# Performance work log

Hardware: AMD Instinct MI355X
Metric: run time of the kernel (lower is better)

The kernel has to match this reference:

```python
import jax, jax.numpy as jnp
import numpy as np

T = 1024          # num tokens
H = 2048          # hidden_size
NH = 16           # attention heads
NKV = 4           # kv heads (GQA)
HD = 128          # head_dim
E = 32            # num routed experts
K = 4             # top_k
I = 1024          # moe_intermediate_size
NS = 1            # num_shared_experts
EPS = 1e-6
THETA = 600000.0  # rope base
SCALE = HD ** -0.5


def rmsnorm(x, w):
    return x * jax.lax.rsqrt(jnp.mean(x * x, axis=-1, keepdims=True) + EPS) * w


def rope(x, positions):
    # x: [T, n_heads, HD], neox-style rotation on full head_dim
    half = HD // 2
    inv_freq = 1.0 / (THETA ** (jnp.arange(half, dtype=jnp.float32) / half))
    ang = positions.astype(jnp.float32)[:, None] * inv_freq        # [T, half]
    cos = jnp.cos(ang)[:, None, :]
    sin = jnp.sin(ang)[:, None, :]
    x1, x2 = x[..., :half], x[..., half:]
    return jnp.concatenate([x1 * cos - x2 * sin, x1 * sin + x2 * cos], axis=-1)


def setup_inputs() -> dict:
    key = jax.random.key(0)
    ks = jax.random.split(key, 10)
    s = 0.02
    return {
        "hidden_states": jax.random.normal(ks[0], (T, H), dtype=jnp.float32),
        "positions": jnp.arange(T, dtype=jnp.int32),
        "w_rms1": jnp.ones((H,), jnp.float32),
        "w_rms2": jnp.ones((H,), jnp.float32),
        "w_qkv": jax.random.normal(ks[1], ((NH + 2 * NKV) * HD, H), jnp.float32) * s,
        "w_o": jax.random.normal(ks[2], (H, NH * HD), jnp.float32) * s,
        "w_router": jax.random.normal(ks[3], (E, H), jnp.float32) * s,
        "w1": jax.random.normal(ks[4], (E, H, I), jnp.float32) * s,   # expert gate proj
        "w3": jax.random.normal(ks[5], (E, H, I), jnp.float32) * s,   # expert up proj
        "w2": jax.random.normal(ks[6], (E, I, H), jnp.float32) * s,   # expert down proj
        "ws_gate_up": jax.random.normal(ks[7], (2 * I * NS, H), jnp.float32) * s,
        "ws_down": jax.random.normal(ks[8], (H, I * NS), jnp.float32) * s,
    }


def reference(hidden_states, positions, w_rms1, w_rms2, w_qkv, w_o, w_router,
              w1, w3, w2, ws_gate_up, ws_down):
    x = hidden_states
    # ---- attention block ----
    h = rmsnorm(x, w_rms1)
    qkv = h @ w_qkv.T                                   # [T, (NH+2NKV)*HD]
    q = qkv[:, : NH * HD].reshape(T, NH, HD)
    k = qkv[:, NH * HD : (NH + NKV) * HD].reshape(T, NKV, HD)
    v = qkv[:, (NH + NKV) * HD :].reshape(T, NKV, HD)
    q = rope(q, positions)
    k = rope(k, positions)
    rep = NH // NKV
    k = jnp.repeat(k, rep, axis=1)                      # [T, NH, HD]
    v = jnp.repeat(v, rep, axis=1)
    scores = jnp.einsum("thd,shd->hts", q, k) * SCALE   # [NH, T, T]
    causal = jnp.tril(jnp.ones((T, T), dtype=bool))
    scores = jnp.where(causal, scores, -jnp.inf)
    attn = jax.nn.softmax(scores, axis=-1)
    o = jnp.einsum("hts,shd->thd", attn, v).reshape(T, NH * HD)
    x = x + o @ w_o.T                                   # residual
    # ---- MoE block ----
    h2 = rmsnorm(x, w_rms2)
    # router in fp32 (router_dtype default)
    logits = h2.astype(jnp.float32) @ w_router.T        # [T, E]
    probs = jax.nn.softmax(logits, axis=-1)
    topv, topi = jax.lax.top_k(probs, K)                # [T, K]
    topv = topv / jnp.sum(topv, axis=-1, keepdims=True)  # norm_topk_prob
    combine = jnp.zeros((T, E), jnp.float32).at[jnp.arange(T)[:, None], topi].add(topv)
    combine = combine.astype(h2.dtype)                  # routed_scaling_factor = 1.0
    g = jnp.einsum("th,ehi->tei", h2, w1)               # [T, E, I]
    u = jnp.einsum("th,ehi->tei", h2, w3)
    a = jax.nn.silu(g) * u                              # SiluAndMul
    d = jnp.einsum("tei,eih->teh", a, w2)               # [T, E, H]
    routed = jnp.einsum("teh,te->th", d, combine)
    # shared expert MLP
    gu = h2 @ ws_gate_up.T                              # [T, 2*I*NS]
    gs, us = gu[:, : I * NS], gu[:, I * NS :]
    shared = (jax.nn.silu(gs) * us) @ ws_down.T
    return x + routed + shared
```

## Files before the change

### kernel.cpp

```cpp
#include <hip/hip_runtime.h>
#include <hip/hip_bf16.h>
#include <math.h>
#include <stdint.h>

#define T_ 1024
#define H_ 2048
#define NH_ 16
#define NKV_ 4
#define HD_ 128
#define E_ 32
#define TOPK_ 4
#define I_ 1024
#define QKVN_ 3072
#define EPS_ 1e-6f
#define THETA_ 600000.0f
#define SCALE_ 0.08838834764831845f

typedef unsigned short u16;
typedef u16 u16x4 __attribute__((ext_vector_type(4)));
typedef u16 u16x8 __attribute__((ext_vector_type(8)));
typedef __bf16 bf16x8 __attribute__((ext_vector_type(8)));
typedef float f32x4 __attribute__((ext_vector_type(4)));

__device__ __forceinline__ u16 f2b(float f) {
  unsigned u = __builtin_bit_cast(unsigned, f);
  u += 0x7FFFu + ((u >> 16) & 1u);
  return (u16)(u >> 16);
}
__device__ __forceinline__ float b2f(u16 x) {
  unsigned u = ((unsigned)x) << 16;
  return __builtin_bit_cast(float, u);
}
__device__ __forceinline__ int s2(int i) { return (i ^ (i >> 2)) & 3; }
__device__ __forceinline__ int sw3(int i) { return (i ^ (i >> 3)) & 7; }

__device__ __forceinline__ void gload16(const void* g, void* l) {
  __builtin_amdgcn_global_load_lds(
      reinterpret_cast<const __attribute__((address_space(1))) unsigned int*>(
          reinterpret_cast<uintptr_t>(g)),
      reinterpret_cast<__attribute__((address_space(3))) unsigned int*>(
          reinterpret_cast<uintptr_t>(l)),
      16, 0, 0);
}

template<int EPI, bool GATHER>
__global__ __launch_bounds__(512, 8) void moe_gemm_k(
    const u16* __restrict__ A, const float* __restrict__ B, const float* __restrict__ B2,
    float* __restrict__ O1, float* __restrict__ O2,
    int NW, int lda, int ldb, int K,
    const int* __restrict__ eoff, const int* __restrict__ tpre,
    const int* __restrict__ slots, const float* __restrict__ slotw, long long sBz)
{
  __shared__ u16 As[2][64 * 64];
  __shared__ u16 Bs[2][64 * 64];

  const int idx = blockIdx.x;
  const int t = idx >> 5;
  const int xx = idx & 31;
  if (t >= tpre[E_]) return;
  int lo = 0, hi = E_;
  while (hi - lo > 1) { int mid = (lo + hi) >> 1; if (tpre[mid] <= t) lo = mid; else hi = mid; }
  const int e = lo;
  const int mb = t - tpre[e];
  const int goff = eoff[e];
  const int Mloc = eoff[e + 1] - goff;
  const int m0 = mb * 64;

  const float* Bp;
  float* Op;
  int n0;
  if constexpr (EPI == 0) {
    int wsel = xx >> 4;
    n0 = (xx & 15) * 64;
    Bp = (wsel ? B2 : B) + (long long)e * sBz;
    Op = wsel ? O2 : O1;
  } else {
    n0 = xx * 64;
    Bp = B + (long long)e * sBz;
    Op = O1;
  }
  const u16* Ae = GATHER ? A : (A + (long long)goff * lda);

  const int tid = threadIdx.x;
  const int lane = tid & 63;
  const int wv = tid >> 6;
  const int wm = wv >> 2, wn = wv & 3;
  const int kg = lane >> 4;
  const int cr = lane & 15;

  const u16* Abase;
  {
    int r = wv * 8 + (lane >> 3);
    int rr = m0 + r;
    if (rr > Mloc - 1) rr = Mloc - 1;
    long long grow = GATHER ? (long long)slots[goff + rr] : (long long)rr;
    Abase = Ae + grow * (long long)lda + (((lane & 7) ^ sw3(r)) << 3);
  }
  auto stageA = [&](int bf, int k0) {
    gload16(Abase + k0, &As[bf][wv * 512]);
  };

  const int bn = tid & 63;
  const int kc = tid >> 6;
  const float* Bbase = Bp + (long long)(kc << 3) * ldb + n0 + bn;
  const int bws = bn * 64 + ((kc ^ sw3(bn)) << 3);

  float br[8];
  auto loadB = [&](int k0) {
    const float* p = Bbase + (long long)k0 * ldb;
    #pragma unroll
    for (int j = 0; j < 8; ++j) br[j] = p[(long long)j * ldb];
  };
  auto writeB = [&](int bf) {
    u16x8 o;
    #pragma unroll
    for (int j = 0; j < 8; ++j) o[j] = f2b(br[j]);
    *(u16x8*)(&Bs[bf][bws]) = o;
  };

  f32x4 acc[2];
  acc[0] = f32x4{0.f, 0.f, 0.f, 0.f};
  acc[1] = f32x4{0.f, 0.f, 0.f, 0.f};

  int aoff[2], asw[2];
  #pragma unroll
  for (int m = 0; m < 2; ++m) {
    int r = wm * 32 + m * 16 + cr;
    aoff[m] = r * 64; asw[m] = sw3(r);
  }
  const int bc = wn * 16 + cr;
  const int boff = bc * 64;
  const int bsw = sw3(bc);

  auto mfma_step = [&](int bf) {
    const u16* Ap = &As[bf][0];
    const u16* Bq = &Bs[bf][0];
    #pragma unroll
    for (int sub = 0; sub < 2; ++sub) {
      int ck = kg + sub * 4;
      bf16x8 af0 = __builtin_bit_cast(bf16x8, *(const u16x8*)(Ap + aoff[0] + ((ck ^ asw[0]) << 3)));
      bf16x8 af1 = __builtin_bit_cast(bf16x8, *(const u16x8*)(Ap + aoff[1] + ((ck ^ asw[1]) << 3)));
      bf16x8 bfr = __builtin_bit_cast(bf16x8, *(const u16x8*)(Bq + boff + ((ck ^ bsw) << 3)));
      acc[0] = __builtin_amdgcn_mfma_f32_16x16x32_bf16(af0, bfr, acc[0], 0, 0, 0);
      acc[1] = __builtin_amdgcn_mfma_f32_16x16x32_bf16(af1, bfr, acc[1], 0, 0, 0);
    }
  };

  loadB(0);
  stageA(0, 0);
  writeB(0);
  __syncthreads();

  int buf = 0;
  for (int ks = 0; ks < K; ks += 64) {
    bool more = (ks + 64) < K;
    if (more) { loadB(ks + 64); stageA(buf ^ 1, ks + 64); }
    mfma_step(buf);
    if (more) writeB(buf ^ 1);
    __syncthreads();
    buf ^= 1;
  }

  const int rq = lane >> 4;
  #pragma unroll
  for (int m = 0; m < 2; ++m) {
    #pragma unroll
    for (int j = 0; j < 4; ++j) {
      int row = m0 + wm * 32 + m * 16 + rq * 4 + j;
      if (row >= Mloc) continue;
      int col = n0 + wn * 16 + cr;
      if constexpr (EPI == 0) {
        Op[(long long)(goff + row) * NW + col] = acc[m][j];
      } else {
        int tok = slots[goff + row];
        float wgt = slotw[goff + row];
        atomicAdd(Op + (long long)tok * NW + col, wgt * acc[m][j]);
      }
    }
  }
}

template<typename TB, int EPI, int CAUSAL>
__global__ __launch_bounds__(512, 8) void dense_gemm_k(
    const u16* __restrict__ A, const TB* __restrict__ B,
    u16* __restrict__ Cb, float* __restrict__ Cf,
    const float* __restrict__ res1, const float* __restrict__ res2,
    int K, int lda, int ldb, int ldc, float alpha,
    long long sAz, long long sBz, long long sCz, int bdivz)
{
  __shared__ u16 As[2][64 * 32];
  __shared__ u16 Bs[2][128 * 32];

  const int m0 = blockIdx.y * 64;
  const int n0 = blockIdx.x * 128;
  if (CAUSAL == 1 && n0 > m0 + 63) return;
  const long long z = blockIdx.z;
  const u16* Ae = A + z * sAz;
  const TB* Be = B + (long long)(z / bdivz) * sBz;
  u16* Cwb = Cb ? Cb + z * sCz : nullptr;

  int kend = K;
  if (CAUSAL == 2) { int ke = m0 + 64; if (ke < kend) kend = ke; }

  const int tid = threadIdx.x;
  const int lane = tid & 63;
  const int wv = tid >> 6;
  const int wm = wv >> 2, wn = wv & 3;

  const u16* Abase = nullptr;
  if (wv < 4) {
    int r = wv * 16 + (lane >> 2);
    Abase = Ae + (long long)(m0 + r) * lda + (((lane & 3) ^ s2(r)) << 3);
  }
  auto stageA = [&](int bf, int k0) {
    if (wv < 4) gload16(Abase + k0, &As[bf][wv * 512]);
  };

  const u16* Bu16base = nullptr;
  const float* Bf32base = nullptr;
  int bws = 0;
  if constexpr (sizeof(TB) == 2) {
    int r = wv * 16 + (lane >> 2);
    Bu16base = (const u16*)Be + (long long)(n0 + r) * ldb + (((lane & 3) ^ s2(r)) << 3);
  } else {
    int bn = tid >> 2, bkq = tid & 3;
    Bf32base = (const float*)Be + (long long)(n0 + bn) * ldb + (bkq << 3);
    bws = bn * 32 + ((bkq ^ s2(bn)) << 3);
  }
  float br[8];
  auto loadB = [&](int k0) {
    const float* p = Bf32base + k0;
    float4 a = *(const float4*)p;
    float4 b = *(const float4*)(p + 4);
    br[0] = a.x; br[1] = a.y; br[2] = a.z; br[3] = a.w;
    br[4] = b.x; br[5] = b.y; br[6] = b.z; br[7] = b.w;
  };
  auto writeB = [&](int bf) {
    u16x8 o;
    #pragma unroll
    for (int j = 0; j < 8; ++j) o[j] = f2b(br[j]);
    *(u16x8*)(&Bs[bf][bws]) = o;
  };
  auto stageBu = [&](int bf, int k0) {
    gload16(Bu16base + k0, &Bs[bf][wv * 512]);
  };

  f32x4 acc[2][2];
  #pragma unroll
  for (int m = 0; m < 2; ++m)
    #pragma unroll
    for (int n = 0; n < 2; ++n)
      acc[m][n] = f32x4{0.f, 0.f, 0.f, 0.f};

  const int kg = lane >> 4;
  const int cr = lane & 15;

  int aoff[2], boff[2];
  #pragma unroll
  for (int m = 0; m < 2; ++m) {
    int r = wm * 32 + m * 16 + cr;
    aoff[m] = r * 32 + ((kg ^ s2(r)) << 3);
  }
  #pragma unroll
  for (int n = 0; n < 2; ++n) {
    int c = wn * 32 + n * 16 + cr;
    boff[n] = c * 32 + ((kg ^ s2(c)) << 3);
  }

  if constexpr (sizeof(TB) == 4) {
    loadB(0); stageA(0, 0); writeB(0);
  } else {
    stageA(0, 0); stageBu(0, 0);
  }
  __syncthreads();

  int buf = 0;
  for (int ks = 0; ks < kend; ks += 32) {
    bool more = (ks + 32) < kend;
    if (more) {
      if constexpr (sizeof(TB) == 4) { loadB(ks + 32); stageA(buf ^ 1, ks + 32); }
      else { stageA(buf ^ 1, ks + 32); stageBu(buf ^ 1, ks + 32); }
    }
    const u16* Ap = &As[buf][0];
    const u16* Bq = &Bs[buf][0];
    bf16x8 af[2], bfr[2];
    #pragma unroll
    for (int m = 0; m < 2; ++m)
      af[m] = __builtin_bit_cast(bf16x8, *(const u16x8*)(Ap + aoff[m]));
    #pragma unroll
    for (int n = 0; n < 2; ++n)
      bfr[n] = __builtin_bit_cast(bf16x8, *(const u16x8*)(Bq + boff[n]));
    #pragma unroll
    for (int m = 0; m < 2; ++m)
      #pragma unroll
      for (int n = 0; n < 2; ++n)
        acc[m][n] = __builtin_amdgcn_mfma_f32_16x16x32_bf16(af[m], bfr[n], acc[m][n], 0, 0, 0);
    if constexpr (sizeof(TB) == 4) { if (more) writeB(buf ^ 1); }
    __syncthreads();
    buf ^= 1;
  }

  const int rq = lane >> 4;
  #pragma unroll
  for (int m = 0; m < 2; ++m) {
    #pragma unroll
    for (int j = 0; j < 4; ++j) {
      int row = m0 + wm * 32 + m * 16 + rq * 4 + j;
      #pragma unroll
      for (int n = 0; n < 2; ++n) {
        int col = n0 + wn * 32 + n * 16 + cr;
        float v = acc[m][n][j];
        long long o = (long long)row * ldc + col;
        if constexpr (EPI == 0) {
          Cwb[o] = f2b(v);
        } else if constexpr (EPI == 1) {
          Cwb[o] = f2b(v * alpha);
        } else if constexpr (EPI == 2) {
          Cf[o] = res1[o] + v;
        } else {
          Cf[o] = res1[o] + res2[o] + v;
        }
      }
    }
  }
}

__global__ __launch_bounds__(256) void vtrans_k(const u16* __restrict__ v_r,
                                                u16* __restrict__ v_t) {
  __shared__ u16 t[64][72];
  int kv = blockIdx.z;
  int s0 = blockIdx.x * 64, d0 = blockIdx.y * 64;
  int tid = threadIdx.x;
  int sr = tid >> 2, dq = (tid & 3) * 16;
  const u16* src = v_r + ((long long)kv * T_ + s0 + sr) * HD_ + d0 + dq;
  *(u16x8*)&t[sr][dq] = *(const u16x8*)src;
  *(u16x8*)&t[sr][dq + 8] = *(const u16x8*)(src + 8);
  __syncthreads();
  int dr = tid >> 2, sq = (tid & 3) * 16;
  u16* dst = v_t + ((long long)kv * HD_ + d0 + dr) * T_ + s0 + sq;
  u16x8 o0, o1;
  #pragma unroll
  for (int j = 0; j < 8; ++j) { o0[j] = t[sq + j][dr]; o1[j] = t[sq + 8 + j][dr]; }
  *(u16x8*)dst = o0;
  *(u16x8*)(dst + 8) = o1;
}

__global__ __launch_bounds__(256) void rmsnorm_k(const float* __restrict__ x,
                                                 const float* __restrict__ w,
                                                 u16* __restrict__ outb,
                                                 float* __restrict__ outf) {
  int t = blockIdx.x;
  int tid = threadIdx.x;
  const float* xr = x + (long long)t * H_;
  float4 a = *(const float4*)(xr + tid * 8);
  float4 b = *(const float4*)(xr + tid * 8 + 4);
  float ss = a.x * a.x + a.y * a.y + a.z * a.z + a.w * a.w +
             b.x * b.x + b.y * b.y + b.z * b.z + b.w * b.w;
  #pragma unroll
  for (int o = 32; o; o >>= 1) ss += __shfl_down(ss, o);
  __shared__ float red[4];
  if ((tid & 63) == 0) red[tid >> 6] = ss;
  __syncthreads();
  float sc = rsqrtf((red[0] + red[1] + red[2] + red[3]) * (1.0f / H_) + EPS_);
  float vo[8] = {a.x, a.y, a.z, a.w, b.x, b.y, b.z, b.w};
  const float* wr = w + tid * 8;
  u16x8 ob;
  #pragma unroll
  for (int q = 0; q < 8; ++q) {
    float val = vo[q] * sc * wr[q];
    ob[q] = f2b(val);
    if (outf) outf[(long long)t * H_ + tid * 8 + q] = val;
  }
  *(u16x8*)(outb + (long long)t * H_ + tid * 8) = ob;
}

__global__ __launch_bounds__(256) void rope_k(const u16* __restrict__ qkv,
                                              const int* __restrict__ pos,
                                              u16* __restrict__ q_r,
                                              u16* __restrict__ k_r,
                                              u16* __restrict__ v_r) {
  int t = blockIdx.x;
  int tid = threadIdx.x;
  float p = (float)pos[t];
  const u16* row = qkv + (long long)t * QKVN_;
  const float cfac = logf(THETA_) * (1.0f / 64.0f);
  #pragma unroll
  for (int it = 0; it < 4; ++it) {
    int item = it * 256 + tid;
    int h = item >> 6, d = item & 63;
    float inv = expf(-cfac * (float)d);
    float ang = p * inv;
    float c = cosf(ang), s = sinf(ang);
    float x1v = b2f(row[h * 128 + d]);
    float x2v = b2f(row[h * 128 + 64 + d]);
    u16* dst = q_r + ((long long)h * T_ + t) * HD_;
    dst[d] = f2b(x1v * c - x2v * s);
    dst[d + 64] = f2b(x1v * s + x2v * c);
  }
  {
    int item = tid;
    int kv = item >> 6, d = item & 63;
    float inv = expf(-cfac * (float)d);
    float ang = p * inv;
    float c = cosf(ang), s = sinf(ang);
    float x1v = b2f(row[NH_ * HD_ + kv * 128 + d]);
    float x2v = b2f(row[NH_ * HD_ + kv * 128 + 64 + d]);
    u16* dst = k_r + ((long long)kv * T_ + t) * HD_;
    dst[d] = f2b(x1v * c - x2v * s);
    dst[d + 64] = f2b(x1v * s + x2v * c);
  }
  #pragma unroll
  for (int it = 0; it < 2; ++it) {
    int item = it * 256 + tid;
    int kv = item >> 7, d = item & 127;
    v_r[((long long)kv * T_ + t) * HD_ + d] = row[(NH_ + NKV_) * HD_ + kv * 128 + d];
  }
}

__global__ __launch_bounds__(64) void softmax_k(u16* __restrict__ P) {
  int r = blockIdx.x;
  int h = r >> 10, i = r & 1023;
  u16* row = P + ((long long)h * T_ + i) * T_;
  int lane = threadIdx.x;
  int n = i + 1;
  float vals[16];
  float mx = -1e30f;
  #pragma unroll
  for (int it = 0; it < 16; ++it) {
    int j = it * 64 + lane;
    float s = (j < n) ? b2f(row[j]) : -1e30f;
    vals[it] = s;
    mx = fmaxf(mx, s);
  }
  #pragma unroll
  for (int o = 32; o; o >>= 1) mx = fmaxf(mx, __shfl_xor(mx, o));
  float sum = 0.f;
  #pragma unroll
  for (int it = 0; it < 16; ++it) {
    int j = it * 64 + lane;
    float e = (j < n) ? __expf(vals[it] - mx) : 0.f;
    vals[it] = e;
    sum += e;
  }
  #pragma unroll
  for (int o = 32; o; o >>= 1) sum += __shfl_xor(sum, o);
  float inv = 1.f / sum;
  #pragma unroll
  for (int it = 0; it < 16; ++it) {
    int j = it * 64 + lane;
    row[j] = f2b(vals[it] * inv);
  }
}

__global__ __launch_bounds__(256) void router2_k(const float* __restrict__ h2,
                                                 const float* __restrict__ wr,
                                                 float* __restrict__ logits) {
  __shared__ float hrow[H_];
  int t = blockIdx.x;
  int tid = threadIdx.x;
  float4 a = *(const float4*)(h2 + (long long)t * H_ + tid * 8);
  float4 b = *(const float4*)(h2 + (long long)t * H_ + tid * 8 + 4);
  *(float4*)&hrow[tid * 8] = a;
  *(float4*)&hrow[tid * 8 + 4] = b;
  __syncthreads();
  int wv = tid >> 6, lane = tid & 63;
  #pragma unroll
  for (int ei = 0; ei < 8; ++ei) {
    int e = wv * 8 + ei;
    const float* wrow = wr + (long long)e * H_;
    float s = 0.f;
    #pragma unroll
    for (int it = 0; it < 8; ++it) {
      int k = it * 256 + lane * 4;
      float4 w4 = *(const float4*)(wrow + k);
      s += hrow[k] * w4.x + hrow[k + 1] * w4.y + hrow[k + 2] * w4.z + hrow[k + 3] * w4.w;
    }
    #pragma unroll
    for (int o = 32; o; o >>= 1) s += __shfl_xor(s, o);
    if (lane == 0) logits[t * E_ + e] = s;
  }
}

__global__ __launch_bounds__(256) void topk_k(const float* __restrict__ logits,
                                              int* __restrict__ topi,
                                              float* __restrict__ topw) {
  int t = blockIdx.x * 256 + threadIdx.x;
  if (t >= T_) return;
  float l[E_];
  #pragma unroll
  for (int e = 0; e < E_; ++e) l[e] = logits[t * E_ + e];
  int sel[TOPK_];
  float sv[TOPK_];
  unsigned used = 0;
  for (int j = 0; j < TOPK_; ++j) {
    float best = -1e30f;
    int bi = 0;
    for (int e = 0; e < E_; ++e) {
      if (used & (1u << e)) continue;
      if (l[e] > best) { best = l[e]; bi = e; }
    }
    used |= 1u << bi;
    sel[j] = bi;
    sv[j] = best;
  }
  float mx = sv[0];
  float s = 0.f;
  #pragma unroll
  for (int j = 0; j < TOPK_; ++j) { sv[j] = __expf(sv[j] - mx); s += sv[j]; }
  float inv = 1.f / s;
  #pragma unroll
  for (int j = 0; j < TOPK_; ++j) {
    topi[t * TOPK_ + j] = sel[j];
    topw[t * TOPK_ + j] = sv[j] * inv;
  }
}

__global__ __launch_bounds__(256) void hist_k(const int* __restrict__ topi, int* __restrict__ cnt) {
  int idx = blockIdx.x * 256 + threadIdx.x;
  if (idx < T_ * TOPK_) atomicAdd(&cnt[topi[idx]], 1);
}

__global__ __launch_bounds__(64) void scan_k(const int* __restrict__ cnt,
                                             int* __restrict__ eoff,
                                             int* __restrict__ cursor,
                                             int* __restrict__ tpre) {
  if (threadIdx.x == 0) {
    int s = 0, tt = 0;
    for (int e = 0; e < E_; ++e) {
      eoff[e] = s; cursor[e] = s; tpre[e] = tt;
      tt += (cnt[e] + 63) >> 6;
      s += cnt[e];
    }
    eoff[E_] = s; tpre[E_] = tt;
  }
}

__global__ __launch_bounds__(256) void scatter_k(const int* __restrict__ topi,
                                                 const float* __restrict__ topw,
                                                 int* __restrict__ cursor,
                                                 int* __restrict__ slots,
                                                 float* __restrict__ slotw) {
  int idx = blockIdx.x * 256 + threadIdx.x;
  if (idx >= T_ * TOPK_) return;
  int e = topi[idx];
  int pos = atomicAdd(&cursor[e], 1);
  slots[pos] = idx >> 2;
  slotw[pos] = topw[idx];
}

__global__ __launch_bounds__(256) void silumul_f_k(const float* __restrict__ g,
                                                   const float* __restrict__ u,
                                                   u16* __restrict__ a) {
  long long idx = ((long long)blockIdx.x * 256 + threadIdx.x) * 8;
  float4 g0 = *(const float4*)(g + idx);
  float4 g1 = *(const float4*)(g + idx + 4);
  float4 u0 = *(const float4*)(u + idx);
  float4 u1 = *(const float4*)(u + idx + 4);
  float gv[8] = {g0.x, g0.y, g0.z, g0.w, g1.x, g1.y, g1.z, g1.w};
  float uv[8] = {u0.x, u0.y, u0.z, u0.w, u1.x, u1.y, u1.z, u1.w};
  u16x8 o;
  #pragma unroll
  for (int q = 0; q < 8; ++q) {
    float x = gv[q];
    float sl = x / (1.f + __expf(-x));
    o[q] = f2b(sl * uv[q]);
  }
  *(u16x8*)(a + idx) = o;
}

__global__ __launch_bounds__(256) void sharedact_k(const u16* __restrict__ gu,
                                                   u16* __restrict__ act) {
  long long idx = ((long long)blockIdx.x * 256 + threadIdx.x) * 8;
  long long t = idx >> 10;
  int i = (int)(idx & 1023);
  const u16* row = gu + t * (2 * I_);
  u16x8 g = *(const u16x8*)(row + i);
  u16x8 u = *(const u16x8*)(row + I_ + i);
  u16x8 o;
  #pragma unroll
  for (int q = 0; q < 8; ++q) {
    float x = b2f(g[q]);
    float y = b2f(u[q]);
    float sl = x / (1.f + __expf(-x));
    o[q] = f2b(sl * y);
  }
  *(u16x8*)(act + t * I_ + i) = o;
}

extern "C" void kernel_launch(void* const* d_in, const int* in_sizes, int n_in,
                              void* d_out, int out_size, void* d_ws, size_t ws_size,
                              hipStream_t stream) {
  const float* x        = (const float*)d_in[0];
  const int* positions  = (const int*)d_in[1];
  const float* w_rms1   = (const float*)d_in[2];
  const float* w_rms2   = (const float*)d_in[3];
  const float* w_qkv    = (const float*)d_in[4];
  const float* w_o      = (const float*)d_in[5];
  const float* w_router = (const float*)d_in[6];
  const float* w1       = (const float*)d_in[7];
  const float* w3       = (const float*)d_in[8];
  const float* w2       = (const float*)d_in[9];
  const float* ws_gu    = (const float*)d_in[10];
  const float* ws_dn    = (const float*)d_in[11];
  float* out = (float*)d_out;

  char* ws = (char*)d_ws;
  size_t off = 0;
  auto alloc = [&](size_t bytes) {
    size_t o = off;
    off = (off + bytes + 255) & ~(size_t)255;
    return (void*)(ws + o);
  };
  u16*  h1b     = (u16*)alloc((size_t)T_ * H_ * 2);
  u16*  qkvb    = (u16*)alloc((size_t)T_ * QKVN_ * 2);
  u16*  q_r     = (u16*)alloc((size_t)NH_ * T_ * HD_ * 2);
  u16*  k_r     = (u16*)alloc((size_t)NKV_ * T_ * HD_ * 2);
  u16*  v_r     = (u16*)alloc((size_t)NKV_ * T_ * HD_ * 2);
  u16*  v_t     = (u16*)alloc((size_t)NKV_ * HD_ * T_ * 2);
  u16*  scoresP = (u16*)alloc((size_t)NH_ * T_ * T_ * 2);
  u16*  o_attn  = (u16*)alloc((size_t)T_ * H_ * 2);
  float* x1     = (float*)alloc((size_t)T_ * H_ * 4);
  float* h2f    = (float*)alloc((size_t)T_ * H_ * 4);
  u16*  h2b     = (u16*)alloc((size_t)T_ * H_ * 2);
  u16*  gub     = (u16*)alloc((size_t)T_ * 2 * I_ * 2);
  u16*  actsh   = (u16*)alloc((size_t)T_ * I_ * 2);
  float* logits = (float*)alloc((size_t)T_ * E_ * 4);
  int*  topi    = (int*)alloc((size_t)T_ * TOPK_ * 4);
  float* topw   = (float*)alloc((size_t)T_ * TOPK_ * 4);
  int*  cnt     = (int*)alloc(E_ * 4);
  int*  eoffp   = (int*)alloc((E_ + 1) * 4);
  int*  cursor  = (int*)alloc(E_ * 4);
  int*  tpre    = (int*)alloc((E_ + 1) * 4);
  int*  slots   = (int*)alloc((size_t)T_ * TOPK_ * 4);
  float* slotw  = (float*)alloc((size_t)T_ * TOPK_ * 4);
  u16*  a_g     = (u16*)alloc((size_t)T_ * TOPK_ * I_ * 2);
  float* routed = (float*)alloc((size_t)T_ * H_ * 4);

  float* g_f32 = (float*)scoresP;
  float* u_f32 = g_f32 + (size_t)T_ * TOPK_ * I_;

  hipMemsetAsync(routed, 0, (size_t)T_ * H_ * 4, stream);
  hipMemsetAsync(cnt, 0, E_ * 4, stream);

  rmsnorm_k<<<T_, 256, 0, stream>>>(x, w_rms1, h1b, nullptr);

  dense_gemm_k<float, 0, 0><<<dim3(24, 16, 1), 512, 0, stream>>>(
      h1b, w_qkv, qkvb, nullptr, nullptr, nullptr,
      H_, H_, H_, QKVN_, 1.f, 0, 0, 0, 1);

  rope_k<<<T_, 256, 0, stream>>>(qkvb, positions, q_r, k_r, v_r);
  vtrans_k<<<dim3(16, 2, 4), 256, 0, stream>>>(v_r, v_t);

  dense_gemm_k<u16, 1, 1><<<dim3(8, 16, NH_), 512, 0, stream>>>(
      q_r, k_r, scoresP, nullptr, nullptr, nullptr,
      HD_, HD_, HD_, T_, SCALE_,
      (long long)T_ * HD_, (long long)T_ * HD_, (long long)T_ * T_, NH_ / NKV_);

  softmax_k<<<NH_ * T_, 64, 0, stream>>>(scoresP);

  dense_gemm_k<u16, 0, 2><<<dim3(1, 16, NH_), 512, 0, stream>>>(
      scoresP, v_t, o_attn, nullptr, nullptr, nullptr,
      T_, T_, T_, H_, 1.f,
      (long long)T_ * T_, (long long)HD_ * T_, (long long)HD_, NH_ / NKV_);

  dense_gemm_k<float, 2, 0><<<dim3(16, 16, 1), 512, 0, stream>>>(
      o_attn, w_o, nullptr, x1, x, nullptr,
      H_, H_, H_, H_, 1.f, 0, 0, 0, 1);

  rmsnorm_k<<<T_, 256, 0, stream>>>(x1, w_rms2, h2b, h2f);

  router2_k<<<T_, 256, 0, stream>>>(h2f, w_router, logits);
  topk_k<<<4, 256, 0, stream>>>(logits, topi, topw);
  hist_k<<<16, 256, 0, stream>>>(topi, cnt);
  scan_k<<<1, 64, 0, stream>>>(cnt, eoffp, cursor, tpre);
  scatter_k<<<16, 256, 0, stream>>>(topi, topw, cursor, slots, slotw);

  moe_gemm_k<0, true><<<3072, 512, 0, stream>>>(
      h2b, w1, w3, g_f32, u_f32,
      I_, H_, I_, H_, eoffp, tpre, slots, nullptr, (long long)H_ * I_);
  silumul_f_k<<<(T_ * TOPK_ * I_) / (256 * 8), 256, 0, stream>>>(g_f32, u_f32, a_g);

  moe_gemm_k<1, false><<<3072, 512, 0, stream>>>(
      a_g, w2, nullptr, routed, nullptr,
      H_, I_, H_, I_, eoffp, tpre, slots, slotw, (long long)I_ * H_);

  dense_gemm_k<float, 0, 0><<<dim3(16, 16, 1), 512, 0, stream>>>(
      h2b, ws_gu, gub, nullptr, nullptr, nullptr,
      H_, H_, H_, 2 * I_, 1.f, 0, 0, 0, 1);
  sharedact_k<<<(T_ * I_) / (256 * 8), 256, 0, stream>>>(gub, actsh);

  dense_gemm_k<float, 4, 0><<<dim3(16, 16, 1), 512, 0, stream>>>(
      actsh, ws_dn, nullptr, out, x1, routed,
      I_, I_, I_, H_, 1.f, 0, 0, 0, 1);
}
```

Before: 585.9 us.

## Fold shared-expert GEMMs into MoE grouped GEMM launches and accumulate directly into output

Adds 512 extra tail blocks to each MoE grouped GEMM that compute the shared-expert gate/up and down projections from transposed row-major weights. The routed and shared down-projection results are atomically accumulated straight into the output. The output is pre-initialised with x1 in the o_proj epilogue, which removes the routed buffer, its memset and the final residual-add GEMM. The aim is fewer launches and more parallel work per launch, at the cost of more float atomics on the output and a more branchy kernel. The non-gather path now adds goff to the row index itself, and the dense EPI 5 branch now falls in the else arm.

```diff
diff --git a/kernel.cpp b/kernel.cpp
--- a/kernel.cpp
+++ b/kernel.cpp
@@ -15,6 +15,7 @@
 #define EPS_ 1e-6f
 #define THETA_ 600000.0f
 #define SCALE_ 0.08838834764831845f
+#define NMOE_ 3072
 
 typedef unsigned short u16;
 typedef u16 u16x4 __attribute__((ext_vector_type(4)));
@@ -49,37 +50,45 @@
     float* __restrict__ O1, float* __restrict__ O2,
     int NW, int lda, int ldb, int K,
     const int* __restrict__ eoff, const int* __restrict__ tpre,
-    const int* __restrict__ slots, const float* __restrict__ slotw, long long sBz)
+    const int* __restrict__ slots, const float* __restrict__ slotw, long long sBz,
+    const u16* __restrict__ Ad, const float* __restrict__ Bd,
+    u16* __restrict__ Od_b, float* __restrict__ Od_f)
 {
   __shared__ u16 As[2][64 * 64];
   __shared__ u16 Bs[2][64 * 64];
 
   const int idx = blockIdx.x;
-  const int t = idx >> 5;
-  const int xx = idx & 31;
-  if (t >= tpre[E_]) return;
-  int lo = 0, hi = E_;
-  while (hi - lo > 1) { int mid = (lo + hi) >> 1; if (tpre[mid] <= t) lo = mid; else hi = mid; }
-  const int e = lo;
-  const int mb = t - tpre[e];
-  const int goff = eoff[e];
-  const int Mloc = eoff[e + 1] - goff;
-  const int m0 = mb * 64;
-
-  const float* Bp;
-  float* Op;
-  int n0;
-  if constexpr (EPI == 0) {
-    int wsel = xx >> 4;
-    n0 = (xx & 15) * 64;
-    Bp = (wsel ? B2 : B) + (long long)e * sBz;
-    Op = wsel ? O2 : O1;
+  const bool tail = idx >= NMOE_;
+
+  int m0, n0, goff = 0, Mloc = T_, e = 0;
+  const float* Bp = nullptr;
+  float* Op = nullptr;
+  if (tail) {
+    int did = idx - NMOE_;
+    m0 = (did >> 5) * 64;
+    n0 = (did & 31) * 64;
   } else {
-    n0 = xx * 64;
-    Bp = B + (long long)e * sBz;
-    Op = O1;
-  }
-  const u16* Ae = GATHER ? A : (A + (long long)goff * lda);
+    const int t = idx >> 5;
+    const int xx = idx & 31;
+    if (t >= tpre[E_]) return;
+    int lo = 0, hi = E_;
+    while (hi - lo > 1) { int mid = (lo + hi) >> 1; if (tpre[mid] <= t) lo = mid; else hi = mid; }
+    e = lo;
+    const int mb = t - tpre[e];
+    goff = eoff[e];
+    Mloc = eoff[e + 1] - goff;
+    m0 = mb * 64;
+    if constexpr (EPI == 0) {
+      int wsel = xx >> 4;
+      n0 = (xx & 15) * 64;
+      Bp = (wsel ? B2 : B) + (long long)e * sBz;
+      Op = wsel ? O2 : O1;
+    } else {
+      n0 = xx * 64;
+      Bp = B + (long long)e * sBz;
+      Op = O1;
+    }
+  }
 
   const int tid = threadIdx.x;
   const int lane = tid & 63;
@@ -91,10 +100,16 @@
   const u16* Abase;
   {
     int r = wv * 8 + (lane >> 3);
-    int rr = m0 + r;
-    if (rr > Mloc - 1) rr = Mloc - 1;
-    long long grow = GATHER ? (long long)slots[goff + rr] : (long long)rr;
-    Abase = Ae + grow * (long long)lda + (((lane & 7) ^ sw3(r)) << 3);
+    if (tail) {
+      Abase = Ad + (long long)(m0 + r) * lda + (((lane & 7) ^ sw3(r)) << 3);
+    } else {
+      int rr = m0 + r;
+      if (rr > Mloc - 1) rr = Mloc - 1;
+      long long grow = GATHER ? (long long)slots[goff + rr] : (long long)(goff + rr);
+      if (GATHER) grow = (long long)slots[goff + rr];
+      else grow = (long long)(goff + rr);
+      Abase = (GATHER ? A : A) + grow * (long long)lda + (((lane & 7) ^ sw3(r)) << 3);
+    }
   }
   auto stageA = [&](int bf, int k0) {
     gload16(Abase + k0, &As[bf][wv * 512]);
@@ -102,14 +117,27 @@
 
   const int bn = tid & 63;
   const int kc = tid >> 6;
-  const float* Bbase = Bp + (long long)(kc << 3) * ldb + n0 + bn;
+  const float* Bbase;
+  if (tail) {
+    Bbase = Bd + (long long)(n0 + bn) * K + (kc << 3);
+  } else {
+    Bbase = Bp + (long long)(kc << 3) * ldb + n0 + bn;
+  }
   const int bws = bn * 64 + ((kc ^ sw3(bn)) << 3);
 
   float br[8];
   auto loadB = [&](int k0) {
-    const float* p = Bbase + (long long)k0 * ldb;
-    #pragma unroll
-    for (int j = 0; j < 8; ++j) br[j] = p[(long long)j * ldb];
+    if (tail) {
+      const float* p = Bbase + k0;
+      float4 a = *(const float4*)p;
+      float4 b = *(const float4*)(p + 4);
+      br[0] = a.x; br[1] = a.y; br[2] = a.z; br[3] = a.w;
+      br[4] = b.x; br[5] = b.y; br[6] = b.z; br[7] = b.w;
+    } else {
+      const float* p = Bbase + (long long)k0 * ldb;
+      #pragma unroll
+      for (int j = 0; j < 8; ++j) br[j] = p[(long long)j * ldb];
+    }
   };
   auto writeB = [&](int bf) {
     u16x8 o;
@@ -167,14 +195,22 @@
     #pragma unroll
     for (int j = 0; j < 4; ++j) {
       int row = m0 + wm * 32 + m * 16 + rq * 4 + j;
-      if (row >= Mloc) continue;
       int col = n0 + wn * 16 + cr;
-      if constexpr (EPI == 0) {
-        Op[(long long)(goff + row) * NW + col] = acc[m][j];
+      if (tail) {
+        if constexpr (EPI == 0) {
+          Od_b[(long long)row * 2048 + col] = f2b(acc[m][j]);
+        } else {
+          atomicAdd(Od_f + (long long)row * 2048 + col, acc[m][j]);
+        }
       } else {
-        int tok = slots[goff + row];
-        float wgt = slotw[goff + row];
-        atomicAdd(Op + (long long)tok * NW + col, wgt * acc[m][j]);
+        if (row >= Mloc) continue;
+        if constexpr (EPI == 0) {
+          Op[(long long)(goff + row) * NW + col] = acc[m][j];
+        } else {
+          int tok = slots[goff + row];
+          float wgt = slotw[goff + row];
+          atomicAdd(Op + (long long)tok * NW + col, wgt * acc[m][j]);
+        }
       }
     }
   }
@@ -183,8 +219,8 @@
 template<typename TB, int EPI, int CAUSAL>
 __global__ __launch_bounds__(512, 8) void dense_gemm_k(
     const u16* __restrict__ A, const TB* __restrict__ B,
-    u16* __restrict__ Cb, float* __restrict__ Cf,
-    const float* __restrict__ res1, const float* __restrict__ res2,
+    u16* __restrict__ Cb, float* __restrict__ Cf, float* __restrict__ Cf2,
+    const float* __restrict__ res1,
     int K, int lda, int ldb, int ldc, float alpha,
     long long sAz, long long sBz, long long sCz, int bdivz)
 {
@@ -318,7 +354,9 @@
         } else if constexpr (EPI == 2) {
           Cf[o] = res1[o] + v;
         } else {
-          Cf[o] = res1[o] + res2[o] + v;
+          float val = res1[o] + v;
+          Cf[o] = val;
+          Cf2[o] = val;
         }
       }
     }
@@ -634,12 +672,10 @@
   int*  slots   = (int*)alloc((size_t)T_ * TOPK_ * 4);
   float* slotw  = (float*)alloc((size_t)T_ * TOPK_ * 4);
   u16*  a_g     = (u16*)alloc((size_t)T_ * TOPK_ * I_ * 2);
-  float* routed = (float*)alloc((size_t)T_ * H_ * 4);
 
   float* g_f32 = (float*)scoresP;
   float* u_f32 = g_f32 + (size_t)T_ * TOPK_ * I_;
 
-  hipMemsetAsync(routed, 0, (size_t)T_ * H_ * 4, stream);
   hipMemsetAsync(cnt, 0, E_ * 4, stream);
 
   rmsnorm_k<<<T_, 256, 0, stream>>>(x, w_rms1, h1b, nullptr);
@@ -663,8 +699,8 @@
       T_, T_, T_, H_, 1.f,
       (long long)T_ * T_, (long long)HD_ * T_, (long long)HD_, NH_ / NKV_);
 
-  dense_gemm_k<float, 2, 0><<<dim3(16, 16, 1), 512, 0, stream>>>(
-      o_attn, w_o, nullptr, x1, x, nullptr,
+  dense_gemm_k<float, 5, 0><<<dim3(16, 16, 1), 512, 0, stream>>>(
+      o_attn, w_o, nullptr, x1, out, x,
       H_, H_, H_, H_, 1.f, 0, 0, 0, 1);
 
   rmsnorm_k<<<T_, 256, 0, stream>>>(x1, w_rms2, h2b, h2f);
@@ -675,21 +711,15 @@
   scan_k<<<1, 64, 0, stream>>>(cnt, eoffp, cursor, tpre);
   scatter_k<<<16, 256, 0, stream>>>(topi, topw, cursor, slots, slotw);
 
-  moe_gemm_k<0, true><<<3072, 512, 0, stream>>>(
+  moe_gemm_k<0, true><<<NMOE_ + 512, 512, 0, stream>>>(
       h2b, w1, w3, g_f32, u_f32,
-      I_, H_, I_, H_, eoffp, tpre, slots, nullptr, (long long)H_ * I_);
+      I_, H_, I_, H_, eoffp, tpre, slots, nullptr, (long long)H_ * I_,
+      h2b, ws_gu, gub, nullptr);
   silumul_f_k<<<(T_ * TOPK_ * I_) / (256 * 8), 256, 0, stream>>>(g_f32, u_f32, a_g);
-
-  moe_gemm_k<1, false><<<3072, 512, 0, stream>>>(
-      a_g, w2, nullptr, routed, nullptr,
-      H_, I_, H_, I_, eoffp, tpre, slots, slotw, (long long)I_ * H_);
-
-  dense_gemm_k<float, 0, 0><<<dim3(16, 16, 1), 512, 0, stream>>>(
-      h2b, ws_gu, gub, nullptr, nullptr, nullptr,
-      H_, H_, H_, 2 * I_, 1.f, 0, 0, 0, 1);
   sharedact_k<<<(T_ * I_) / (256 * 8), 256, 0, stream>>>(gub, actsh);
 
-  dense_gemm_k<float, 4, 0><<<dim3(16, 16, 1), 512, 0, stream>>>(
-      actsh, ws_dn, nullptr, out, x1, routed,
-      I_, I_, I_, H_, 1.f, 0, 0, 0, 1);
-}
+  moe_gemm_k<1, false><<<NMOE_ + 512, 512, 0, stream>>>(
+      a_g, w2, nullptr, out, nullptr,
+      H_, I_, H_, I_, eoffp, tpre, slots, slotw, (long long)I_ * H_,
+      actsh, ws_dn, nullptr, out);
+}
```

After: 725.1 us. 23.8% more time.

## Accumulate routed and shared expert outputs directly into output; vectorize softmax

Applied to the files above, without the earlier changes.

The o-proj epilogue now writes the residual sum to both x1 and the final output buffer. The routed-expert down projection and the shared-expert down projection then atomically add straight into the output. This removes the separate routed buffer, its memset, and the extra residual reads in the final GEMM. Softmax now handles four rows per block with 8-wide vector loads and stores. The cost is atomic traffic on the shared-down GEMM and a duplicated write of the residual.

```diff
diff --git a/kernel.cpp b/kernel.cpp
--- a/kernel.cpp
+++ b/kernel.cpp
@@ -183,8 +183,8 @@
 template<typename TB, int EPI, int CAUSAL>
 __global__ __launch_bounds__(512, 8) void dense_gemm_k(
     const u16* __restrict__ A, const TB* __restrict__ B,
-    u16* __restrict__ Cb, float* __restrict__ Cf,
-    const float* __restrict__ res1, const float* __restrict__ res2,
+    u16* __restrict__ Cb, float* __restrict__ Cf, float* __restrict__ Cf2,
+    const float* __restrict__ res1,
     int K, int lda, int ldb, int ldc, float alpha,
     long long sAz, long long sBz, long long sCz, int bdivz)
 {
@@ -317,8 +317,12 @@
           Cwb[o] = f2b(v * alpha);
         } else if constexpr (EPI == 2) {
           Cf[o] = res1[o] + v;
+        } else if constexpr (EPI == 5) {
+          float val = res1[o] + v;
+          Cf[o] = val;
+          Cf2[o] = val;
         } else {
-          Cf[o] = res1[o] + res2[o] + v;
+          atomicAdd(&Cf[o], v);
         }
       }
     }
@@ -417,38 +421,48 @@
   }
 }
 
-__global__ __launch_bounds__(64) void softmax_k(u16* __restrict__ P) {
-  int r = blockIdx.x;
+__global__ __launch_bounds__(256) void softmax2_k(u16* __restrict__ P) {
+  int wv = threadIdx.x >> 6, lane = threadIdx.x & 63;
+  int r = blockIdx.x * 4 + wv;
   int h = r >> 10, i = r & 1023;
   u16* row = P + ((long long)h * T_ + i) * T_;
-  int lane = threadIdx.x;
   int n = i + 1;
-  float vals[16];
+  float v[16];
   float mx = -1e30f;
   #pragma unroll
-  for (int it = 0; it < 16; ++it) {
-    int j = it * 64 + lane;
-    float s = (j < n) ? b2f(row[j]) : -1e30f;
-    vals[it] = s;
-    mx = fmaxf(mx, s);
+  for (int c = 0; c < 2; ++c) {
+    int j0 = (c * 64 + lane) * 8;
+    u16x8 xv = *(const u16x8*)(row + j0);
+    #pragma unroll
+    for (int q = 0; q < 8; ++q) {
+      float s = (j0 + q < n) ? b2f(xv[q]) : -1e30f;
+      v[c * 8 + q] = s;
+      mx = fmaxf(mx, s);
+    }
   }
   #pragma unroll
   for (int o = 32; o; o >>= 1) mx = fmaxf(mx, __shfl_xor(mx, o));
   float sum = 0.f;
   #pragma unroll
-  for (int it = 0; it < 16; ++it) {
-    int j = it * 64 + lane;
-    float e = (j < n) ? __expf(vals[it] - mx) : 0.f;
-    vals[it] = e;
-    sum += e;
+  for (int c = 0; c < 2; ++c) {
+    #pragma unroll
+    for (int q = 0; q < 8; ++q) {
+      int j = (c * 64 + lane) * 8 + q;
+      float e = (j < n) ? __expf(v[c * 8 + q] - mx) : 0.f;
+      v[c * 8 + q] = e;
+      sum += e;
+    }
   }
   #pragma unroll
   for (int o = 32; o; o >>= 1) sum += __shfl_xor(sum, o);
   float inv = 1.f / sum;
   #pragma unroll
-  for (int it = 0; it < 16; ++it) {
-    int j = it * 64 + lane;
-    row[j] = f2b(vals[it] * inv);
+  for (int c = 0; c < 2; ++c) {
+    int j0 = (c * 64 + lane) * 8;
+    u16x8 ov;
+    #pragma unroll
+    for (int q = 0; q < 8; ++q) ov[q] = f2b(v[c * 8 + q] * inv);
+    *(u16x8*)(row + j0) = ov;
   }
 }
 
@@ -634,12 +648,10 @@
   int*  slots   = (int*)alloc((size_t)T_ * TOPK_ * 4);
   float* slotw  = (float*)alloc((size_t)T_ * TOPK_ * 4);
   u16*  a_g     = (u16*)alloc((size_t)T_ * TOPK_ * I_ * 2);
-  float* routed = (float*)alloc((size_t)T_ * H_ * 4);
 
   float* g_f32 = (float*)scoresP;
   float* u_f32 = g_f32 + (size_t)T_ * TOPK_ * I_;
 
-  hipMemsetAsync(routed, 0, (size_t)T_ * H_ * 4, stream);
   hipMemsetAsync(cnt, 0, E_ * 4, stream);
 
   rmsnorm_k<<<T_, 256, 0, stream>>>(x, w_rms1, h1b, nullptr);
@@ -656,15 +668,15 @@
       HD_, HD_, HD_, T_, SCALE_,
       (long long)T_ * HD_, (long long)T_ * HD_, (long long)T_ * T_, NH_ / NKV_);
 
-  softmax_k<<<NH_ * T_, 64, 0, stream>>>(scoresP);
+  softmax2_k<<<NH_ * T_ / 4, 256, 0, stream>>>(scoresP);
 
   dense_gemm_k<u16, 0, 2><<<dim3(1, 16, NH_), 512, 0, stream>>>(
       scoresP, v_t, o_attn, nullptr, nullptr, nullptr,
       T_, T_, T_, H_, 1.f,
       (long long)T_ * T_, (long long)HD_ * T_, (long long)HD_, NH_ / NKV_);
 
-  dense_gemm_k<float, 2, 0><<<dim3(16, 16, 1), 512, 0, stream>>>(
-      o_attn, w_o, nullptr, x1, x, nullptr,
+  dense_gemm_k<float, 5, 0><<<dim3(16, 16, 1), 512, 0, stream>>>(
+      o_attn, w_o, nullptr, x1, out, x,
       H_, H_, H_, H_, 1.f, 0, 0, 0, 1);
 
   rmsnorm_k<<<T_, 256, 0, stream>>>(x1, w_rms2, h2b, h2f);
@@ -680,16 +692,16 @@
       I_, H_, I_, H_, eoffp, tpre, slots, nullptr, (long long)H_ * I_);
   silumul_f_k<<<(T_ * TOPK_ * I_) / (256 * 8), 256, 0, stream>>>(g_f32, u_f32, a_g);
 
-  moe_gemm_k<1, false><<<3072, 512, 0, stream>>>(
-      a_g, w2, nullptr, routed, nullptr,
-      H_, I_, H_, I_, eoffp, tpre, slots, slotw, (long long)I_ * H_);
-
   dense_gemm_k<float, 0, 0><<<dim3(16, 16, 1), 512, 0, stream>>>(
       h2b, ws_gu, gub, nullptr, nullptr, nullptr,
       H_, H_, H_, 2 * I_, 1.f, 0, 0, 0, 1);
   sharedact_k<<<(T_ * I_) / (256 * 8), 256, 0, stream>>>(gub, actsh);
 
-  dense_gemm_k<float, 4, 0><<<dim3(16, 16, 1), 512, 0, stream>>>(
-      actsh, ws_dn, nullptr, out, x1, routed,
+  moe_gemm_k<1, false><<<3072, 512, 0, stream>>>(
+      a_g, w2, nullptr, out, nullptr,
+      H_, I_, H_, I_, eoffp, tpre, slots, slotw, (long long)I_ * H_);
+
+  dense_gemm_k<float, 6, 0><<<dim3(16, 16, 1), 512, 0, stream>>>(
+      actsh, ws_dn, nullptr, out, nullptr, nullptr,
       I_, I_, I_, H_, 1.f, 0, 0, 0, 1);
 }
```

Result: no change. 581.4 us (median of 2 runs) (-0.8%).
